# Optimization experiments

Hardware: AMD Instinct MI355X
Metric: run time of the kernel (lower is better)

Reference implementation:

```python
import jax, jax.numpy as jnp
import numpy as np

D, K, S, H, MID, OUT = 1024, 1024, 1000, 16, 4096, 1000
HD = K // H
EPS = 1e-5


def _posenc(d_model, length):
    pos = jnp.arange(length, dtype=jnp.float32)[:, None]              # [S,1]
    div = jnp.exp(jnp.arange(0, d_model, 2, dtype=jnp.float32) * (-np.log(10000.0) / d_model))
    ang = pos * div                                                   # [S,D/2]
    # interleave sin/cos -> pe[:,0::2]=sin, pe[:,1::2]=cos
    return jnp.stack([jnp.sin(ang), jnp.cos(ang)], axis=-1).reshape(length, d_model)


def _ln2d(x):
    # LayerNorm over last two dims (n_seq, d_dim), no affine
    m = jnp.mean(x, axis=(-2, -1), keepdims=True)
    v = jnp.var(x, axis=(-2, -1), keepdims=True)
    return (x - m) * jax.lax.rsqrt(v + EPS)


def setup_inputs() -> dict:
    key = jax.random.key(0)
    ks = jax.random.split(key, 9)
    sc = lambda fan: 1.0 / np.sqrt(fan)
    return {
        "x":   jax.random.normal(ks[0], (8, S, D), dtype=jnp.float32),
        "Wq":  jax.random.normal(ks[1], (D, K), dtype=jnp.float32) * sc(D),
        "Wk":  jax.random.normal(ks[2], (D, K), dtype=jnp.float32) * sc(D),
        "Wv":  jax.random.normal(ks[3], (D, K), dtype=jnp.float32) * sc(D),
        "Wo":  jax.random.normal(ks[4], (K, D), dtype=jnp.float32) * sc(K),
        "W1":  jax.random.normal(ks[5], (D, MID), dtype=jnp.float32) * sc(D),
        "b1":  jnp.zeros((MID,), dtype=jnp.float32),
        "W2":  jax.random.normal(ks[6], (MID, D), dtype=jnp.float32) * sc(MID),
        "b2":  jnp.zeros((D,), dtype=jnp.float32),
        "Wout": jax.random.normal(ks[7], (D, OUT), dtype=jnp.float32) * sc(D),
    }


def reference(x, Wq, Wk, Wv, Wo, W1, b1, W2, b2, Wout):
    B = x.shape[0]
    x = x + _posenc(D, S)                                   # positional add
    # QKV projections -> [B,H,S,HD]
    def heads(w):
        return jnp.einsum('bsd,dk->bsk', x, w).reshape(B, S, H, HD).transpose(0, 2, 1, 3)
    qs, ksv, vs = heads(Wq), heads(Wk), heads(Wv)
    scaling = HD ** (-0.5)
    scores = jnp.einsum('bhsd,bhtd->bhst', qs, ksv) * scaling
    attn = jax.nn.softmax(scores, axis=-1)
    ctx = jnp.einsum('bhst,bhtd->bhsd', attn, vs)
    ctx = ctx.transpose(0, 2, 1, 3).reshape(B, S, K)
    attn_out = _ln2d(jnp.einsum('bsk,kd->bsd', ctx, Wo))    # per-sample LN over (S,D)
    # FFN with residual + LN over (S,D)
    h = jax.nn.relu(jnp.einsum('bsd,dm->bsm', attn_out, W1) + b1)
    f = jnp.einsum('bsm,md->bsd', h, W2) + b2
    ffn = _ln2d(f + attn_out)
    pooled = jnp.mean(ffn, axis=-2)                         # [B,D]
    return jnp.einsum('bd,do->bo', pooled, Wout)            # [B,OUT]
```

## Files before the change

### kernel.cpp

```cpp
#include <hip/hip_runtime.h>
#include <stdint.h>
#include <math.h>

#define DD 1024
#define SS 1000
#define BB 8
#define HH 16
#define MIDD 4096
#define OUTD 1000

typedef unsigned short u16;
typedef __attribute__((ext_vector_type(4))) float f32x4;
typedef __attribute__((ext_vector_type(4))) unsigned int u32x4;

__device__ __forceinline__ u16 f2b(float f) {
    union { float f; uint32_t u; } v; v.f = f;
    uint32_t r = v.u + 0x7fffu + ((v.u >> 16) & 1u);
    return (u16)(r >> 16);
}
__device__ __forceinline__ float b2f(u16 b) {
    union { uint32_t u; float f; } v; v.u = ((uint32_t)b) << 16; return v.f;
}

__device__ __forceinline__ int sz64(int row, int e) {
    return row * 64 + ((((e >> 3) ^ row) & 7) << 3) + (e & 7);
}

__device__ __forceinline__ void mfma_b16(f32x4& d, u32x4 a, u32x4 b) {
    asm("v_mfma_f32_16x16x32_bf16 %0, %1, %2, %0" : "+v"(d) : "v"(a), "v"(b));
}
#define MFMA_FENCE() do { __builtin_amdgcn_sched_barrier(0); \
    asm volatile("s_nop 7\n\ts_nop 7\n\ts_nop 7" ::); \
    __builtin_amdgcn_sched_barrier(0); } while (0)

#define GLDS16(gp, lp) \
    __builtin_amdgcn_global_load_lds((const __attribute__((address_space(1))) uint32_t*)(gp), \
                                     (__attribute__((address_space(3))) uint32_t*)(lp), 16, 0, 0)

__global__ void k_posenc(const float* __restrict__ x, u16* __restrict__ xpe) {
    long p = (long)blockIdx.x * 256 + threadIdx.x;
    if (p >= (long)BB * SS * DD / 2) return;
    int dp = (int)(p & (DD / 2 - 1));
    int s = (int)((p >> 9) % SS);
    float dv = __expf((float)(2 * dp) * (-9.210340371976184f / (float)DD));
    float sn, cs;
    sincosf((float)s * dv, &sn, &cs);
    float2 xv = *(const float2*)&x[p * 2];
    uint32_t pk = (uint32_t)f2b(xv.x + sn) | ((uint32_t)f2b(xv.y + cs) << 16);
    ((uint32_t*)xpe)[p] = pk;
}

__global__ void k_wt(const float* __restrict__ W, u16* __restrict__ Wt, int R, int C, float scale) {
    __shared__ float tile[32][33];
    int bc = blockIdx.x * 32, br = blockIdx.y * 32;
    int tx = threadIdx.x, ty = threadIdx.y;
#pragma unroll
    for (int i = 0; i < 32; i += 8)
        tile[ty + i][tx] = W[(long)(br + ty + i) * C + bc + tx];
    __syncthreads();
#pragma unroll
    for (int i = 0; i < 32; i += 8)
        Wt[(long)(bc + ty + i) * R + br + tx] = f2b(tile[tx][ty + i] * scale);
}

template<int MODE>
__global__ __launch_bounds__(512)
void k_gemm(const u16* __restrict__ A, const u16* __restrict__ Bt, void* __restrict__ Cp,
            const float* __restrict__ bias, const u16* res,
            int M, int N, int K, int lda, int ldb, int ldc, int ntiles)
{
    __shared__ u16 SA[3][128 * 64];
    __shared__ u16 SB[3][256 * 64];
    const int t = threadIdx.x, lane = t & 63, w = t >> 6;
    const int lr = lane & 15, g = lane >> 4;
    const int wm = w >> 2, wn = w & 3;

    const int orig = blockIdx.x, nwg = gridDim.x;
    const int q8 = nwg >> 3, r8 = nwg & 7, xc = orig & 7;
    const int wg = (xc < r8 ? xc * (q8 + 1) : r8 * (q8 + 1) + (xc - r8) * q8) + (orig >> 3);
    const int bm = (wg / ntiles) * 128, bn = (wg % ntiles) * 256;

    const int srow8 = lane >> 3;
    const int csrc = ((lane & 7) ^ srow8) << 3;
    const u16* ga[2];
    const u16* gb[4];
#pragma unroll
    for (int l = 0; l < 2; ++l) {
        int r = bm + w * 16 + l * 8 + srow8;
        if (r >= M) r = M - 1;
        ga[l] = A + (long)r * lda + csrc;
    }
#pragma unroll
    for (int l = 0; l < 4; ++l)
        gb[l] = Bt + (long)(bn + w * 32 + l * 8 + srow8) * ldb + csrc;

#define STAGE(buf, k0) do { \
        _Pragma("unroll") \
        for (int l = 0; l < 2; ++l) \
            GLDS16(ga[l] + (k0), &SA[buf][(w * 16 + l * 8) * 64]); \
        _Pragma("unroll") \
        for (int l = 0; l < 4; ++l) \
            GLDS16(gb[l] + (k0), &SB[buf][(w * 32 + l * 8) * 64]); \
    } while (0)

    f32x4 acc[4][4] = {};

#define PH(buf, kk) do { \
        u32x4 av[4], bv[4]; \
        _Pragma("unroll") \
        for (int m = 0; m < 4; ++m) \
            av[m] = *(const u32x4*)&SA[buf][sz64(wm * 64 + m * 16 + lr, (kk) * 32 + g * 8)]; \
        _Pragma("unroll") \
        for (int n = 0; n < 4; ++n) \
            bv[n] = *(const u32x4*)&SB[buf][sz64(wn * 64 + n * 16 + lr, (kk) * 32 + g * 8)]; \
        __builtin_amdgcn_s_setprio(1); \
        _Pragma("unroll") \
        for (int m = 0; m < 4; ++m) \
            _Pragma("unroll") \
            for (int n = 0; n < 4; ++n) \
                mfma_b16(acc[m][n], av[m], bv[n]); \
        __builtin_amdgcn_s_setprio(0); \
    } while (0)

    const int nt = K >> 6;

    STAGE(0, 0);
    STAGE(1, 64);

    int cb = 0, sb = 2;
    for (int tt = 0; tt < nt; ++tt) {
        if (tt + 1 < nt) asm volatile("s_waitcnt vmcnt(6)" ::: "memory");
        else             asm volatile("s_waitcnt vmcnt(0)" ::: "memory");
        __builtin_amdgcn_s_barrier();
        if (tt + 2 < nt) STAGE(sb, (tt + 2) << 6);
        PH(cb, 0);
        PH(cb, 1);
        cb = (cb == 2) ? 0 : cb + 1;
        sb = (sb == 2) ? 0 : sb + 1;
    }
#undef PH
#undef STAGE

    MFMA_FENCE();

#pragma unroll
    for (int m = 0; m < 4; ++m) {
#pragma unroll
        for (int j = 0; j < 4; ++j) {
            const int r = bm + wm * 64 + m * 16 + g * 4 + j;
            if (r >= M) continue;
            const long ro = (long)r * ldc;
#pragma unroll
            for (int n = 0; n < 4; ++n) {
                const int c = bn + wn * 64 + n * 16 + lr;
                float v = acc[m][n][j];
                if (MODE == 0)      ((float*)Cp)[ro + c] = v;
                else if (MODE == 1) ((u16*)Cp)[ro + c] = f2b(v);
                else if (MODE == 2) { v += bias[c]; ((u16*)Cp)[ro + c] = f2b(v > 0.f ? v : 0.f); }
                else                { v += bias[c] + b2f(res[ro + c]); ((u16*)Cp)[ro + c] = f2b(v); }
            }
        }
    }
}

__global__ void k_vt(const u16* __restrict__ QKV, u16* __restrict__ Vt) {
    __shared__ u16 tile[128][80];
    int b = blockIdx.z, h = blockIdx.y, s0 = blockIdx.x * 128;
    int t = threadIdx.x;
    int rr = t >> 3, cc = (t & 7) * 8;
#pragma unroll
    for (int p = 0; p < 4; ++p) {
        int s = s0 + p * 32 + rr;
        uint4 val = make_uint4(0u, 0u, 0u, 0u);
        if (s < SS) val = *(const uint4*)&QKV[((long)(b * SS + s)) * 3072 + 2048 + h * 64 + cc];
        *(uint4*)&tile[p * 32 + rr][cc] = val;
    }
    __syncthreads();
    int d = t >> 2, sg = (t & 3) * 32;
    long base = ((long)((b * HH + h) * 64 + d)) * 1024 + s0 + sg;
#pragma unroll
    for (int i = 0; i < 4; ++i) {
        u16 tmp[8];
#pragma unroll
        for (int jj = 0; jj < 8; ++jj) tmp[jj] = tile[sg + i * 8 + jj][d];
        *(uint4*)&Vt[base + i * 8] = *(uint4*)tmp;
    }
}

__global__ __launch_bounds__(256)
void k_flash(const u16* __restrict__ QKV, const u16* __restrict__ Vt, u16* __restrict__ ctx)
{
    __shared__ u16 Ps[128 * 64];
    __shared__ u16 Ks[64 * 64];
    __shared__ u16 Vs[64 * 64];
    __shared__ u16 Vones[16 * 64];
    const int t = threadIdx.x, lane = t & 63, wave = t >> 6;
    const int lr = lane & 15, g = lane >> 4;
    const int f = blockIdx.x;
    const int bh = (f & 7) + ((f >> 6) << 3);
    const int q0 = ((f >> 3) & 7) * 128;
    const int h = bh & 15, b = bh >> 4;
    const u16* Qg = QKV + (long)b * SS * 3072 + h * 64;
    const u16* Kg = Qg + 1024;
    const u16* Vg = Vt + (long)bh * 65536;

    const int sr8 = wave * 8 + (lane >> 3);
    const int ssrc = ((lane & 7) ^ (lane >> 3)) * 8;
    const int ldst0 = sr8 * 64 + (lane & 7) * 8;
    const int ldst1 = (32 + sr8) * 64 + (lane & 7) * 8;

#pragma unroll
    for (int r = 0; r < 4; ++r) {
        int qr = q0 + r * 32 + sr8; if (qr >= SS) qr = SS - 1;
        GLDS16(Qg + (long)qr * 3072 + ssrc, &Ps[(r * 32 + wave * 8) * 64]);
    }

    u32x4 kr0, kr1, vr0, vr1;
    {
        kr0 = *(const u32x4*)(Kg + (long)sr8 * 3072 + ssrc);
        kr1 = *(const u32x4*)(Kg + (long)(32 + sr8) * 3072 + ssrc);
        vr0 = *(const u32x4*)(Vg + (long)sr8 * 1024 + ssrc);
        vr1 = *(const u32x4*)(Vg + (long)(32 + sr8) * 1024 + ssrc);
    }

    __syncthreads();
    u32x4 qa[2][2];
#pragma unroll
    for (int m = 0; m < 2; ++m)
#pragma unroll
        for (int ks = 0; ks < 2; ++ks)
            qa[m][ks] = *(const u32x4*)&Ps[sz64(wave * 32 + m * 16 + lr, ks * 32 + g * 8)];

    *(u32x4*)&Ks[ldst0] = kr0;
    *(u32x4*)&Ks[ldst1] = kr1;
    *(u32x4*)&Vs[ldst0] = vr0;
    *(u32x4*)&Vs[ldst1] = vr1;
    for (int i = t; i < 16 * 64; i += 256)
        Vones[sz64(i >> 6, i & 63)] = ((i >> 6) == 0) ? (u16)0x3F80 : (u16)0;
    __syncthreads();

    f32x4 o[2][5] = {};

    for (int tt = 0; tt < 16; ++tt) {
        const int kt = tt * 64;
        if (tt < 15) {
            int a0 = kt + 64 + sr8;      if (a0 >= SS) a0 = SS - 1;
            int a1 = kt + 64 + 32 + sr8; if (a1 >= SS) a1 = SS - 1;
            kr0 = *(const u32x4*)(Kg + (long)a0 * 3072 + ssrc);
            kr1 = *(const u32x4*)(Kg + (long)a1 * 3072 + ssrc);
            vr0 = *(const u32x4*)(Vg + (long)sr8 * 1024 + kt + 64 + ssrc);
            vr1 = *(const u32x4*)(Vg + (long)(32 + sr8) * 1024 + kt + 64 + ssrc);
        }

        f32x4 s[2][4] = {};
#pragma unroll
        for (int ks = 0; ks < 2; ++ks) {
            u32x4 kb[4];
#pragma unroll
            for (int n = 0; n < 4; ++n)
                kb[n] = *(const u32x4*)&Ks[sz64(n * 16 + lr, ks * 32 + g * 8)];
            __builtin_amdgcn_s_setprio(1);
#pragma unroll
            for (int m = 0; m < 2; ++m)
#pragma unroll
                for (int n = 0; n < 4; ++n)
                    mfma_b16(s[m][n], qa[m][ks], kb[n]);
            __builtin_amdgcn_s_setprio(0);
        }
        MFMA_FENCE();

        if (tt == 15) {
#pragma unroll
            for (int n = 0; n < 4; ++n) {
                const bool oob = (kt + n * 16 + lr) >= SS;
                if (oob)
#pragma unroll
                    for (int m = 0; m < 2; ++m)
#pragma unroll
                        for (int j = 0; j < 4; ++j) s[m][n][j] = -1e30f;
            }
        }

#pragma unroll
        for (int m = 0; m < 2; ++m)
#pragma unroll
            for (int j = 0; j < 4; ++j) {
                float p0 = exp2f(s[m][0][j]);
                float p1 = exp2f(s[m][1][j]);
                float p2 = exp2f(s[m][2][j]);
                float p3 = exp2f(s[m][3][j]);
                uint32_t pk01, pk23;
                asm("v_cvt_pk_bf16_f32 %0, %1, %2" : "=v"(pk01) : "v"(p0), "v"(p1));
                asm("v_cvt_pk_bf16_f32 %0, %1, %2" : "=v"(pk23) : "v"(p2), "v"(p3));
                const int prow = wave * 32 + m * 16 + g * 4 + j;
                Ps[sz64(prow, 0 * 16 + lr)] = (u16)(pk01 & 0xffff);
                Ps[sz64(prow, 1 * 16 + lr)] = (u16)(pk01 >> 16);
                Ps[sz64(prow, 2 * 16 + lr)] = (u16)(pk23 & 0xffff);
                Ps[sz64(prow, 3 * 16 + lr)] = (u16)(pk23 >> 16);
            }

        asm volatile("s_waitcnt lgkmcnt(0)" ::: "memory");
        __builtin_amdgcn_sched_barrier(0);

#pragma unroll
        for (int m = 0; m < 2; ++m) {
            u32x4 pa0 = *(const u32x4*)&Ps[sz64(wave * 32 + m * 16 + lr, g * 8)];
            u32x4 pa1 = *(const u32x4*)&Ps[sz64(wave * 32 + m * 16 + lr, 32 + g * 8)];
            __builtin_amdgcn_s_setprio(1);
#pragma unroll
            for (int nd = 0; nd < 4; ++nd) {
                u32x4 vb0 = *(const u32x4*)&Vs[sz64(nd * 16 + lr, g * 8)];
                u32x4 vb1 = *(const u32x4*)&Vs[sz64(nd * 16 + lr, 32 + g * 8)];
                mfma_b16(o[m][nd], pa0, vb0);
                mfma_b16(o[m][nd], pa1, vb1);
            }
            {
                u32x4 vb0 = *(const u32x4*)&Vones[sz64(lr, g * 8)];
                u32x4 vb1 = *(const u32x4*)&Vones[sz64(lr, 32 + g * 8)];
                mfma_b16(o[m][4], pa0, vb0);
                mfma_b16(o[m][4], pa1, vb1);
            }
            __builtin_amdgcn_s_setprio(0);
        }

        if (tt < 15) {
            __syncthreads();
            *(u32x4*)&Ks[ldst0] = kr0;
            *(u32x4*)&Ks[ldst1] = kr1;
            *(u32x4*)&Vs[ldst0] = vr0;
            *(u32x4*)&Vs[ldst1] = vr1;
            __syncthreads();
        }
    }

    MFMA_FENCE();

#pragma unroll
    for (int m = 0; m < 2; ++m)
#pragma unroll
        for (int j = 0; j < 4; ++j) {
            const int r = q0 + wave * 32 + m * 16 + g * 4 + j;
            if (r >= SS) continue;
            const float lval = __shfl(o[m][4][j], lane & 48);
            const float inv = 1.0f / lval;
#pragma unroll
            for (int nd = 0; nd < 4; ++nd)
                ctx[((long)b * SS + r) * 1024 + h * 64 + nd * 16 + lr] = f2b(o[m][nd][j] * inv);
        }
}

__global__ void k_stats1b(const u16* __restrict__ X, float* __restrict__ part) {
    int b = blockIdx.y, blk = blockIdx.x, t = threadIdx.x;
    const uint4* xp = (const uint4*)(X + (long)b * (SS * DD));
    float s = 0.f, q = 0.f;
    for (int i = blk * 256 + t; i < SS * DD / 8; i += 128 * 256) {
        uint4 v = xp[i];
        uint32_t w[4] = { v.x, v.y, v.z, v.w };
#pragma unroll
        for (int jj = 0; jj < 4; ++jj) {
            float a = b2f((u16)(w[jj] & 0xffff)), c = b2f((u16)(w[jj] >> 16));
            s += a + c; q += a * a + c * c;
        }
    }
#pragma unroll
    for (int o = 32; o; o >>= 1) { s += __shfl_xor(s, o, 64); q += __shfl_xor(q, o, 64); }
    __shared__ float rs[4], rq[4];
    if ((t & 63) == 0) { rs[t >> 6] = s; rq[t >> 6] = q; }
    __syncthreads();
    if (t == 0) {
        part[(b * 128 + blk) * 2]     = rs[0] + rs[1] + rs[2] + rs[3];
        part[(b * 128 + blk) * 2 + 1] = rq[0] + rq[1] + rq[2] + rq[3];
    }
}

__global__ void k_stats2(const float* __restrict__ part, float* __restrict__ st) {
    int b = blockIdx.x, t = threadIdx.x;
    float s = part[(b * 128 + t) * 2], q = part[(b * 128 + t) * 2 + 1];
#pragma unroll
    for (int o = 32; o; o >>= 1) { s += __shfl_xor(s, o, 64); q += __shfl_xor(q, o, 64); }
    __shared__ float rs[2], rq[2];
    if ((t & 63) == 0) { rs[t >> 6] = s; rq[t >> 6] = q; }
    __syncthreads();
    if (t == 0) {
        float sm = rs[0] + rs[1], sq = rq[0] + rq[1];
        float mean = sm / (float)(SS * DD);
        float var = sq / (float)(SS * DD) - mean * mean;
        st[b * 2] = mean;
        st[b * 2 + 1] = rsqrtf(var + 1e-5f);
    }
}

__global__ void k_lnapplyb(const u16* __restrict__ X, const float* __restrict__ st,
                           u16* __restrict__ ob) {
    int b = blockIdx.y;
    long i = (long)b * (SS * DD) + ((long)blockIdx.x * 256 + threadIdx.x) * 8;
    const float mean = st[b * 2], rstd = st[b * 2 + 1];
    uint4 v = *(const uint4*)&X[i];
    uint32_t w[4] = { v.x, v.y, v.z, v.w };
    uint32_t r[4];
#pragma unroll
    for (int jj = 0; jj < 4; ++jj) {
        float a = (b2f((u16)(w[jj] & 0xffff)) - mean) * rstd;
        float c = (b2f((u16)(w[jj] >> 16)) - mean) * rstd;
        r[jj] = (uint32_t)f2b(a) | ((uint32_t)f2b(c) << 16);
    }
    *(uint4*)&ob[i] = make_uint4(r[0], r[1], r[2], r[3]);
}

__global__ void k_colpool1(const u16* __restrict__ F, float* __restrict__ partc) {
    int dg = blockIdx.x, sc = blockIdx.y, b = blockIdx.z;
    int d = dg * 256 + threadIdx.x;
    const u16* fp = F + (long)b * (SS * DD) + (long)sc * 125 * DD + d;
    float s = 0.f;
#pragma unroll 5
    for (int i = 0; i < 125; ++i) s += b2f(fp[(long)i * DD]);
    partc[((b * 8 + sc) * DD) + d] = s;
}
__global__ void k_colpool2(const float* __restrict__ partc, const float* __restrict__ st,
                           float* __restrict__ pooled) {
    int b = blockIdx.y, d = blockIdx.x * 256 + threadIdx.x;
    float s = 0.f;
#pragma unroll
    for (int c = 0; c < 8; ++c) s += partc[(b * 8 + c) * DD + d];
    pooled[b * DD + d] = (s * (1.0f / SS) - st[b * 2]) * st[b * 2 + 1];
}

__global__ void k_out1(const float* __restrict__ pooled, const float* __restrict__ Wout,
                       float* __restrict__ po) {
    const int og = blockIdx.x, dc = blockIdx.y, t = threadIdx.x;
    const int o = og * 256 + t;
    __shared__ float pl[8][32];
    pl[t >> 5][t & 31] = pooled[(t >> 5) * DD + dc * 32 + (t & 31)];
    __syncthreads();
    if (o >= OUTD) return;
    float acc[8] = {};
    for (int i = 0; i < 32; ++i) {
        float wv = Wout[(long)(dc * 32 + i) * OUTD + o];
#pragma unroll
        for (int bb = 0; bb < 8; ++bb) acc[bb] = fmaf(pl[bb][i], wv, acc[bb]);
    }
#pragma unroll
    for (int bb = 0; bb < 8; ++bb) po[(dc * 8 + bb) * OUTD + o] = acc[bb];
}
__global__ void k_out2(const float* __restrict__ po, float* __restrict__ out) {
    int b = blockIdx.y, o = blockIdx.x * 256 + threadIdx.x;
    if (o >= OUTD) return;
    float s = 0.f;
    for (int c = 0; c < 32; ++c) s += po[(c * 8 + b) * OUTD + o];
    out[b * OUTD + o] = s;
}

extern "C" void kernel_launch(void* const* d_in, const int* in_sizes, int n_in,
                              void* d_out, int out_size, void* d_ws, size_t ws_size,
                              hipStream_t stream) {
    const float* x    = (const float*)d_in[0];
    const float* Wq   = (const float*)d_in[1];
    const float* Wk   = (const float*)d_in[2];
    const float* Wv   = (const float*)d_in[3];
    const float* Wo   = (const float*)d_in[4];
    const float* W1   = (const float*)d_in[5];
    const float* b1   = (const float*)d_in[6];
    const float* W2   = (const float*)d_in[7];
    const float* b2   = (const float*)d_in[8];
    const float* Wout = (const float*)d_in[9];
    float* out = (float*)d_out;

    char* base = (char*)d_ws;
    u16*   xpe    = (u16*)(base);
    u16*   ctx    = xpe;
    u16*   attnb  = xpe;
    u16*   fout   = xpe;
    u16*   QKVb   = (u16*)(base + 16384000);
    u16*   hb     = QKVb;
    u16*   Vt     = (u16*)(base + 65536000);
    u16*   aob    = Vt;
    float* partc  = (float*)(base + 65536000);
    float* po     = (float*)(base + 65536000 + 262144);
    char*  wbase  = base + 82313216;
    u16*   Wqkvt  = (u16*)(wbase);
    u16*   Wot    = (u16*)(wbase + 6291456);
    u16*   W1t    = (u16*)(wbase + 8388608);
    u16*   W2t    = (u16*)(wbase + 16777216);
    char*  mbase  = base + 107479040;
    float* part   = (float*)(mbase);
    float* st1    = (float*)(mbase + 8192);
    float* st2    = (float*)(mbase + 8448);
    float* pooled = (float*)(mbase + 8704);

    const float CEXP = 0.18033688f;

    dim3 blk(256);
    k_posenc<<<dim3(16000), blk, 0, stream>>>(x, xpe);
    k_wt<<<dim3(32, 32), dim3(32, 8), 0, stream>>>(Wq, Wqkvt, 1024, 1024, CEXP);
    k_wt<<<dim3(32, 32), dim3(32, 8), 0, stream>>>(Wk, Wqkvt + 1048576, 1024, 1024, 1.f);
    k_wt<<<dim3(32, 32), dim3(32, 8), 0, stream>>>(Wv, Wqkvt + 2097152, 1024, 1024, 1.f);
    k_wt<<<dim3(32, 32), dim3(32, 8), 0, stream>>>(Wo, Wot, 1024, 1024, 1.f);
    k_wt<<<dim3(128, 32), dim3(32, 8), 0, stream>>>(W1, W1t, 1024, 4096, 1.f);
    k_wt<<<dim3(32, 128), dim3(32, 8), 0, stream>>>(W2, W2t, 4096, 1024, 1.f);

    k_gemm<1><<<dim3(756), dim3(512), 0, stream>>>(xpe, Wqkvt, QKVb, nullptr, nullptr,
                                                   8000, 3072, 1024, 1024, 1024, 3072, 12);
    k_vt<<<dim3(8, 16, 8), blk, 0, stream>>>(QKVb, Vt);

    k_flash<<<dim3(1024), blk, 0, stream>>>(QKVb, Vt, ctx);

    k_gemm<1><<<dim3(252), dim3(512), 0, stream>>>(ctx, Wot, aob, nullptr, nullptr,
                                                   8000, 1024, 1024, 1024, 1024, 1024, 4);
    k_stats1b<<<dim3(128, 8), blk, 0, stream>>>(aob, part);
    k_stats2<<<dim3(8), dim3(128), 0, stream>>>(part, st1);
    k_lnapplyb<<<dim3(500, 8), blk, 0, stream>>>(aob, st1, attnb);

    k_gemm<2><<<dim3(1008), dim3(512), 0, stream>>>(attnb, W1t, hb, b1, nullptr,
                                                    8000, 4096, 1024, 1024, 1024, 4096, 16);
    k_gemm<3><<<dim3(252), dim3(512), 0, stream>>>(hb, W2t, fout, b2, attnb,
                                                   8000, 1024, 4096, 4096, 4096, 1024, 4);

    k_stats1b<<<dim3(128, 8), blk, 0, stream>>>(fout, part);
    k_stats2<<<dim3(8), dim3(128), 0, stream>>>(part, st2);
    k_colpool1<<<dim3(4, 8, 8), blk, 0, stream>>>(fout, partc);
    k_colpool2<<<dim3(4, 8), blk, 0, stream>>>(partc, st2, pooled);
    k_out1<<<dim3(4, 32), blk, 0, stream>>>(pooled, Wout, po);
    k_out2<<<dim3(4, 8), blk, 0, stream>>>(po, out);
}
```

Baseline: 447.0 us.

## Add 256-row GEMM tile with double-buffered split staging and M-fast tile ordering

Templates the GEMM on the M tile size and on tile traversal order. The W1 GEMM now uses 256x256 tiles with two LDS buffers: A is staged ahead of the barrier and B is staged between the two MFMA phases. The W1 and W2 GEMMs also walk tiles with M as the fast index, so consecutive workgroups share the same weight columns. The aim is more MFMA work per LDS and global load and better L2 reuse of weights, at the cost of more accumulator registers, shallower prefetch and fewer workgroups.

```diff
diff --git a/kernel.cpp b/kernel.cpp
--- a/kernel.cpp
+++ b/kernel.cpp
@@ -63,14 +63,17 @@
         Wt[(long)(bc + ty + i) * R + br + tx] = f2b(tile[tx][ty + i] * scale);
 }
 
-template<int MODE>
+template<int MODE, int BM, bool NFAST>
 __global__ __launch_bounds__(512)
 void k_gemm(const u16* __restrict__ A, const u16* __restrict__ Bt, void* __restrict__ Cp,
             const float* __restrict__ bias, const u16* res,
-            int M, int N, int K, int lda, int ldb, int ldc, int ntiles)
+            int M, int N, int K, int lda, int ldb, int ldc, int tiles)
 {
-    __shared__ u16 SA[3][128 * 64];
-    __shared__ u16 SB[3][256 * 64];
+    constexpr int MF = BM / 32;
+    constexpr int AL = BM / 64;
+    constexpr int NBUF = (BM == 128) ? 3 : 2;
+    __shared__ u16 SA[NBUF][BM * 64];
+    __shared__ u16 SB[NBUF][256 * 64];
     const int t = threadIdx.x, lane = t & 63, w = t >> 6;
     const int lr = lane & 15, g = lane >> 4;
     const int wm = w >> 2, wn = w & 3;
@@ -78,15 +81,16 @@
     const int orig = blockIdx.x, nwg = gridDim.x;
     const int q8 = nwg >> 3, r8 = nwg & 7, xc = orig & 7;
     const int wg = (xc < r8 ? xc * (q8 + 1) : r8 * (q8 + 1) + (xc - r8) * q8) + (orig >> 3);
-    const int bm = (wg / ntiles) * 128, bn = (wg % ntiles) * 256;
+    const int bm = (NFAST ? wg / tiles : wg % tiles) * BM;
+    const int bn = (NFAST ? wg % tiles : wg / tiles) * 256;
 
     const int srow8 = lane >> 3;
     const int csrc = ((lane & 7) ^ srow8) << 3;
-    const u16* ga[2];
+    const u16* ga[AL];
     const u16* gb[4];
 #pragma unroll
-    for (int l = 0; l < 2; ++l) {
-        int r = bm + w * 16 + l * 8 + srow8;
+    for (int l = 0; l < AL; ++l) {
+        int r = bm + w * (BM / 8) + l * 8 + srow8;
         if (r >= M) r = M - 1;
         ga[l] = A + (long)r * lda + csrc;
     }
@@ -94,28 +98,30 @@
     for (int l = 0; l < 4; ++l)
         gb[l] = Bt + (long)(bn + w * 32 + l * 8 + srow8) * ldb + csrc;
 
-#define STAGE(buf, k0) do { \
+#define STAGE_A(buf, k0) do { \
         _Pragma("unroll") \
-        for (int l = 0; l < 2; ++l) \
-            GLDS16(ga[l] + (k0), &SA[buf][(w * 16 + l * 8) * 64]); \
+        for (int l = 0; l < AL; ++l) \
+            GLDS16(ga[l] + (k0), &SA[buf][(w * (BM / 8) + l * 8) * 64]); \
+    } while (0)
+#define STAGE_B(buf, k0) do { \
         _Pragma("unroll") \
         for (int l = 0; l < 4; ++l) \
             GLDS16(gb[l] + (k0), &SB[buf][(w * 32 + l * 8) * 64]); \
     } while (0)
 
-    f32x4 acc[4][4] = {};
+    f32x4 acc[MF][4] = {};
 
 #define PH(buf, kk) do { \
-        u32x4 av[4], bv[4]; \
+        u32x4 av[MF], bv[4]; \
         _Pragma("unroll") \
-        for (int m = 0; m < 4; ++m) \
-            av[m] = *(const u32x4*)&SA[buf][sz64(wm * 64 + m * 16 + lr, (kk) * 32 + g * 8)]; \
+        for (int m = 0; m < MF; ++m) \
+            av[m] = *(const u32x4*)&SA[buf][sz64(wm * (BM / 2) + m * 16 + lr, (kk) * 32 + g * 8)]; \
         _Pragma("unroll") \
         for (int n = 0; n < 4; ++n) \
             bv[n] = *(const u32x4*)&SB[buf][sz64(wn * 64 + n * 16 + lr, (kk) * 32 + g * 8)]; \
         __builtin_amdgcn_s_setprio(1); \
         _Pragma("unroll") \
-        for (int m = 0; m < 4; ++m) \
+        for (int m = 0; m < MF; ++m) \
             _Pragma("unroll") \
             for (int n = 0; n < 4; ++n) \
                 mfma_b16(acc[m][n], av[m], bv[n]); \
@@ -124,30 +130,48 @@
 
     const int nt = K >> 6;
 
-    STAGE(0, 0);
-    STAGE(1, 64);
-
-    int cb = 0, sb = 2;
-    for (int tt = 0; tt < nt; ++tt) {
-        if (tt + 1 < nt) asm volatile("s_waitcnt vmcnt(6)" ::: "memory");
-        else             asm volatile("s_waitcnt vmcnt(0)" ::: "memory");
-        __builtin_amdgcn_s_barrier();
-        if (tt + 2 < nt) STAGE(sb, (tt + 2) << 6);
-        PH(cb, 0);
-        PH(cb, 1);
-        cb = (cb == 2) ? 0 : cb + 1;
-        sb = (sb == 2) ? 0 : sb + 1;
+    if constexpr (NBUF == 3) {
+        STAGE_A(0, 0); STAGE_B(0, 0);
+        STAGE_A(1, 64); STAGE_B(1, 64);
+        int cb = 0, sb = 2;
+        for (int tt = 0; tt < nt; ++tt) {
+            if (tt + 1 < nt) asm volatile("s_waitcnt vmcnt(6)" ::: "memory");
+            else             asm volatile("s_waitcnt vmcnt(0)" ::: "memory");
+            __builtin_amdgcn_s_barrier();
+            if (tt + 2 < nt) { STAGE_A(sb, (tt + 2) << 6); STAGE_B(sb, (tt + 2) << 6); }
+            PH(cb, 0);
+            PH(cb, 1);
+            cb = (cb == 2) ? 0 : cb + 1;
+            sb = (sb == 2) ? 0 : sb + 1;
+        }
+    } else {
+        STAGE_A(0, 0); STAGE_B(0, 0);
+        for (int tt = 0; tt < nt; ++tt) {
+            const int cb2 = tt & 1, nb = cb2 ^ 1, kn = (tt + 1) << 6;
+            if (tt + 1 < nt) {
+                STAGE_A(nb, kn);
+                asm volatile("s_waitcnt vmcnt(4)" ::: "memory");
+            } else {
+                asm volatile("s_waitcnt vmcnt(0)" ::: "memory");
+            }
+            __builtin_amdgcn_s_barrier();
+            PH(cb2, 0);
+            if (tt + 1 < nt) STAGE_B(nb, kn);
+            PH(cb2, 1);
+            __builtin_amdgcn_s_barrier();
+        }
     }
 #undef PH
-#undef STAGE
+#undef STAGE_A
+#undef STAGE_B
 
     MFMA_FENCE();
 
 #pragma unroll
-    for (int m = 0; m < 4; ++m) {
+    for (int m = 0; m < MF; ++m) {
 #pragma unroll
         for (int j = 0; j < 4; ++j) {
-            const int r = bm + wm * 64 + m * 16 + g * 4 + j;
+            const int r = bm + wm * (BM / 2) + m * 16 + g * 4 + j;
             if (r >= M) continue;
             const long ro = (long)r * ldc;
 #pragma unroll
@@ -498,22 +522,22 @@
     k_wt<<<dim3(128, 32), dim3(32, 8), 0, stream>>>(W1, W1t, 1024, 4096, 1.f);
     k_wt<<<dim3(32, 128), dim3(32, 8), 0, stream>>>(W2, W2t, 4096, 1024, 1.f);
 
-    k_gemm<1><<<dim3(756), dim3(512), 0, stream>>>(xpe, Wqkvt, QKVb, nullptr, nullptr,
-                                                   8000, 3072, 1024, 1024, 1024, 3072, 12);
+    k_gemm<1, 128, true><<<dim3(756), dim3(512), 0, stream>>>(xpe, Wqkvt, QKVb, nullptr, nullptr,
+                                                              8000, 3072, 1024, 1024, 1024, 3072, 12);
     k_vt<<<dim3(8, 16, 8), blk, 0, stream>>>(QKVb, Vt);
 
     k_flash<<<dim3(1024), blk, 0, stream>>>(QKVb, Vt, ctx);
 
-    k_gemm<1><<<dim3(252), dim3(512), 0, stream>>>(ctx, Wot, aob, nullptr, nullptr,
-                                                   8000, 1024, 1024, 1024, 1024, 1024, 4);
+    k_gemm<1, 128, true><<<dim3(252), dim3(512), 0, stream>>>(ctx, Wot, aob, nullptr, nullptr,
+                                                              8000, 1024, 1024, 1024, 1024, 1024, 4);
     k_stats1b<<<dim3(128, 8), blk, 0, stream>>>(aob, part);
     k_stats2<<<dim3(8), dim3(128), 0, stream>>>(part, st1);
     k_lnapplyb<<<dim3(500, 8), blk, 0, stream>>>(aob, st1, attnb);
 
-    k_gemm<2><<<dim3(1008), dim3(512), 0, stream>>>(attnb, W1t, hb, b1, nullptr,
-                                                    8000, 4096, 1024, 1024, 1024, 4096, 16);
-    k_gemm<3><<<dim3(252), dim3(512), 0, stream>>>(hb, W2t, fout, b2, attnb,
-                                                   8000, 1024, 4096, 4096, 4096, 1024, 4);
+    k_gemm<2, 256, false><<<dim3(512), dim3(512), 0, stream>>>(attnb, W1t, hb, b1, nullptr,
+                                                               8000, 4096, 1024, 1024, 1024, 4096, 32);
+    k_gemm<3, 128, false><<<dim3(252), dim3(512), 0, stream>>>(hb, W2t, fout, b2, attnb,
+                                                               8000, 1024, 4096, 4096, 4096, 1024, 63);
 
     k_stats1b<<<dim3(128, 8), blk, 0, stream>>>(fout, part);
     k_stats2<<<dim3(8), dim3(128), 0, stream>>>(part, st2);
```

After: 435.3 us. 2.6% less time.
